# Kernel tuning notes

Measured on AMD Instinct MI355X. Metric: run time of the kernel, lower is better.

## Reference

```python
import jax, jax.numpy as jnp
import numpy as np

S = 1024      # sequence length
V = 32000     # vocab size
H = 1024      # hidden_dim
A = 128       # attn_size (module default)


def lstm_cell(x, h, c, Wih, Whh, b):
    # torch LSTM gate order: i, f, g, o
    g = x @ Wih.T + h @ Whh.T + b
    i, f, gg, o = jnp.split(g, 4)
    c = jax.nn.sigmoid(f) * c + jax.nn.sigmoid(i) * jnp.tanh(gg)
    h = jax.nn.sigmoid(o) * jnp.tanh(c)
    return h, c


def setup_inputs() -> dict:
    key = jax.random.key(0)
    ks = jax.random.split(key, 16)
    p = lambda k, shape: (jax.random.normal(k, shape, jnp.float32) * 0.02)
    return {
        'input_seq': jax.random.randint(ks[0], (S,), 0, V),
        'gold_seq': jax.random.randint(ks[1], (S,), 0, V),
        'embed': p(ks[2], (V, H)),
        'enc_Wih': p(ks[3], (4 * H, H)),
        'enc_Whh': p(ks[4], (4 * H, H)),
        'enc_b': jnp.zeros((4 * H,), jnp.float32),   # b_ih + b_hh combined
        'dec_Wih': p(ks[5], (4 * H, 2 * H)),          # decoder input = [prev, context]
        'dec_Whh': p(ks[6], (4 * H, H)),
        'dec_b': jnp.zeros((4 * H,), jnp.float32),
        'U_w': p(ks[7], (A, H)), 'U_b': jnp.zeros((A,), jnp.float32),
        'Wa_w': p(ks[8], (A, H)), 'Wa_b': jnp.zeros((A,), jnp.float32),
        'Va_w': p(ks[9], (1, A)), 'Va_b': jnp.zeros((1,), jnp.float32),
        'out_w': p(ks[10], (V, H)), 'out_b': jnp.zeros((V,), jnp.float32),
    }


def reference(input_seq, gold_seq, embed, enc_Wih, enc_Whh, enc_b,
              dec_Wih, dec_Whh, dec_b, U_w, U_b, Wa_w, Wa_b, Va_w, Va_b,
              out_w, out_b):
    Hd = embed.shape[1]
    x_emb = embed[input_seq]  # (S, H)

    def enc_step(carry, x):
        h, c = carry
        h, c = lstm_cell(x, h, c, enc_Wih, enc_Whh, enc_b)
        return (h, c), h

    zero = jnp.zeros((Hd,), x_emb.dtype)
    (h0, c0), enc_out = jax.lax.scan(enc_step, (zero, zero), x_emb)  # enc_out: (S, H)

    U_enc = enc_out @ U_w.T + U_b  # (S, A), hidden-independent part of additive attention

    # teacher forcing: prev_0 = zeros, prev_i = embed(gold[i-1]); relu applied each step
    prev = jnp.concatenate([jnp.zeros((1, Hd), x_emb.dtype), embed[gold_seq[:-1]]], axis=0)
    prev = jax.nn.relu(prev)  # (S, H)

    def dec_step(carry, p):
        h, c = carry
        # additive attention scores: V(tanh(U(enc) + W(h)))  -> (S, 1)
        scores = jnp.tanh(U_enc + h @ Wa_w.T + Wa_b) @ Va_w.T + Va_b
        # faithful to nn.Softmax() on a (S,1) tensor: torch picks dim=1 -> all ones
        w = jax.nn.softmax(scores, axis=1)  # (S, 1), == ones
        context = w[:, 0] @ enc_out         # (H,) == sum of encoder outputs
        x = jnp.concatenate([p, context])   # (2H,)
        h, c = lstm_cell(x, h, c, dec_Wih, dec_Whh, dec_b)
        logits = h @ out_w.T + out_b        # (V,)
        return (h, c), (logits, jnp.argmax(logits))

    _, (preds, idxs) = jax.lax.scan(dec_step, (h0, c0), prev)
    return preds, idxs  # (S, V) float logits, (S,) predicted ids
```

## Files before the change

kernel.cpp:

```cpp
#include <hip/hip_runtime.h>
#include <math.h>


#define S_LEN 1024
#define HDIM  1024
#define VDIM  32000

typedef float f4 __attribute__((ext_vector_type(4)));

__device__ __forceinline__ void agent_storef(float* p, float v) {
    __hip_atomic_store(p, v, __ATOMIC_RELAXED, __HIP_MEMORY_SCOPE_AGENT);
}
__device__ __forceinline__ float sigmoidf_(float x) {
    return 1.0f / (1.0f + expf(-x));
}
__device__ __forceinline__ void llc_load_4x4(const float* p, f4& a, f4& b,
                                             f4& c, f4& d) {
    asm volatile(
        "global_load_dwordx4 %0, %4, off sc0 sc1\n\t"
        "global_load_dwordx4 %1, %4, off offset:1024 sc0 sc1\n\t"
        "global_load_dwordx4 %2, %4, off offset:2048 sc0 sc1\n\t"
        "global_load_dwordx4 %3, %4, off offset:3072 sc0 sc1\n\t"
        "s_waitcnt vmcnt(0)"
        : "=&v"(a), "=&v"(b), "=&v"(c), "=&v"(d)
        : "v"(p) : "memory");
}
__device__ __forceinline__ int swz(int s) {
    return (s & ~7) | ((s ^ (s >> 3)) & 7);
}

template<int MODE>
__global__ __launch_bounds__(256)
void gemm_nt(const float* __restrict__ A, int lda,
             const float* __restrict__ B, int ldb,
             const float* __restrict__ bias,
             float* __restrict__ C, int ldc,
             const float* __restrict__ embed,
             const int* __restrict__ gidx,
             int M, int N, int K)
{
    __shared__ float As[16][128];
    __shared__ float Bs[16][128];

    const int tid = threadIdx.x;
    const int m0 = blockIdx.y * 128;
    const int n0 = blockIdx.x * 128;

    float acc[8][8];
#pragma unroll
    for (int r = 0; r < 8; ++r)
#pragma unroll
        for (int c = 0; c < 8; ++c) acc[r][c] = 0.0f;

    const int ty = tid >> 4;
    const int tx = tid & 15;

    for (int k0 = 0; k0 < K; k0 += 16) {
#pragma unroll
        for (int q = 0; q < 2; ++q) {
            int id = tid * 2 + q;
            int m  = id >> 2;
            int c4 = (id & 3) * 4;
            float4 v;
            if (MODE == 0) {
                v = *(const float4*)(A + (size_t)(m0 + m) * lda + k0 + c4);
            } else if (MODE == 1) {
                int row = gidx[m0 + m];
                v = *(const float4*)(embed + (size_t)row * HDIM + k0 + c4);
            } else {
                int mg = m0 + m;
                if (mg == 0) {
                    v = make_float4(0.f, 0.f, 0.f, 0.f);
                } else {
                    int row = gidx[mg - 1];
                    v = *(const float4*)(embed + (size_t)row * HDIM + k0 + c4);
                    v.x = fmaxf(v.x, 0.f); v.y = fmaxf(v.y, 0.f);
                    v.z = fmaxf(v.z, 0.f); v.w = fmaxf(v.w, 0.f);
                }
            }
            As[c4 + 0][m] = v.x; As[c4 + 1][m] = v.y;
            As[c4 + 2][m] = v.z; As[c4 + 3][m] = v.w;
        }
#pragma unroll
        for (int q = 0; q < 2; ++q) {
            int id = tid * 2 + q;
            int n  = id >> 2;
            int c4 = (id & 3) * 4;
            float4 v = *(const float4*)(B + (size_t)(n0 + n) * ldb + k0 + c4);
            Bs[c4 + 0][n] = v.x; Bs[c4 + 1][n] = v.y;
            Bs[c4 + 2][n] = v.z; Bs[c4 + 3][n] = v.w;
        }
        __syncthreads();

#pragma unroll
        for (int k = 0; k < 16; ++k) {
            float4 a0 = *(const float4*)&As[k][ty * 8];
            float4 a1 = *(const float4*)&As[k][ty * 8 + 4];
            float4 b0 = *(const float4*)&Bs[k][tx * 8];
            float4 b1 = *(const float4*)&Bs[k][tx * 8 + 4];
            float av[8] = {a0.x,a0.y,a0.z,a0.w,a1.x,a1.y,a1.z,a1.w};
            float bv[8] = {b0.x,b0.y,b0.z,b0.w,b1.x,b1.y,b1.z,b1.w};
#pragma unroll
            for (int r = 0; r < 8; ++r)
#pragma unroll
                for (int c = 0; c < 8; ++c)
                    acc[r][c] = fmaf(av[r], bv[c], acc[r][c]);
        }
        __syncthreads();
    }

    const int mbase = m0 + ty * 8;
    const int nbase = n0 + tx * 8;
#pragma unroll
    for (int r = 0; r < 8; ++r) {
        float4 o0, o1;
        o0.x = acc[r][0] + bias[nbase + 0];
        o0.y = acc[r][1] + bias[nbase + 1];
        o0.z = acc[r][2] + bias[nbase + 2];
        o0.w = acc[r][3] + bias[nbase + 3];
        o1.x = acc[r][4] + bias[nbase + 4];
        o1.y = acc[r][5] + bias[nbase + 5];
        o1.z = acc[r][6] + bias[nbase + 6];
        o1.w = acc[r][7] + bias[nbase + 7];
        *(float4*)(C + (size_t)(mbase + r) * ldc + nbase)     = o0;
        *(float4*)(C + (size_t)(mbase + r) * ldc + nbase + 4) = o1;
    }
}

__global__ __launch_bounds__(512, 2)
void lstm_seq(const float* __restrict__ Whh,
              const float* __restrict__ G,
              const float* __restrict__ h_init,
              const float* __restrict__ c_init,
              float* __restrict__ h_out,
              float* __restrict__ c_fin,
              float* __restrict__ csum_out,
              int slen)
{
    __shared__ f4 hbuf[256];
    const int tid = threadIdx.x;
    const int g   = blockIdx.x;
    const int wv  = tid >> 6;
    const int lg  = tid & 63;
    const int j   = g * 8 + wv;

    f4 W[4][4];
#pragma unroll
    for (int q = 0; q < 4; ++q)
#pragma unroll
        for (int i = 0; i < 4; ++i)
            W[q][i] = *(const f4*)(Whh + (size_t)(j + q * HDIM) * HDIM
                                   + 4 * lg + 256 * i);

    float c = 0.0f, csum = 0.0f;
    if (lg == 0) c = c_init[j];

    float gnow = G[(size_t)(lg & 3) * HDIM + j];

    for (int t = 0; t < slen; ++t) {
#pragma unroll
        for (int q = 0; q < 4; ++q)
#pragma unroll
            for (int i = 0; i < 4; ++i)
                asm volatile("" : "+v"(W[q][i]));

        const float* hp = (t == 0) ? h_init : (h_out + (size_t)(t - 1) * HDIM);

        if (wv == 0) {
            f4 a, b, cc, d;
            const float* p = hp + 4 * lg;
            for (;;) {
                llc_load_4x4(p, a, b, cc, d);
                float s0 = (a.x + a.y) + (a.z + a.w);
                float s1 = (b.x + b.y) + (b.z + b.w);
                float s2 = (cc.x + cc.y) + (cc.z + cc.w);
                float s3 = (d.x + d.y) + (d.z + d.w);
                float s  = (s0 + s1) + (s2 + s3);
                if (!__any(s != s)) break;
                __builtin_amdgcn_s_sleep(1);
            }
            hbuf[swz(lg)]       = a;
            hbuf[swz(64 + lg)]  = b;
            hbuf[swz(128 + lg)] = cc;
            hbuf[swz(192 + lg)] = d;
        }
        __syncthreads();

        int tn = (t + 1 < slen) ? (t + 1) : t;
        float gnext = G[(size_t)tn * (4 * HDIM) + (lg & 3) * HDIM + j];

        f4 h0 = hbuf[swz(lg)];
        f4 h1 = hbuf[swz(64 + lg)];
        f4 h2 = hbuf[swz(128 + lg)];
        f4 h3 = hbuf[swz(192 + lg)];
        float p0 = 0.f, p1 = 0.f, p2 = 0.f, p3 = 0.f;
        f4 hv;
#pragma unroll
        for (int i = 0; i < 4; ++i) {
            hv = (i == 0) ? h0 : (i == 1) ? h1 : (i == 2) ? h2 : h3;
            p0 = fmaf(W[0][i].x, hv.x, fmaf(W[0][i].y, hv.y,
                 fmaf(W[0][i].z, hv.z, fmaf(W[0][i].w, hv.w, p0))));
            p1 = fmaf(W[1][i].x, hv.x, fmaf(W[1][i].y, hv.y,
                 fmaf(W[1][i].z, hv.z, fmaf(W[1][i].w, hv.w, p1))));
            p2 = fmaf(W[2][i].x, hv.x, fmaf(W[2][i].y, hv.y,
                 fmaf(W[2][i].z, hv.z, fmaf(W[2][i].w, hv.w, p2))));
            p3 = fmaf(W[3][i].x, hv.x, fmaf(W[3][i].y, hv.y,
                 fmaf(W[3][i].z, hv.z, fmaf(W[3][i].w, hv.w, p3))));
        }

        float t01 = __shfl_xor((lg & 1) ? p0 : p1, 1);
        float s01 = ((lg & 1) ? p1 : p0) + t01;
        float t23 = __shfl_xor((lg & 1) ? p2 : p3, 1);
        float s23 = ((lg & 1) ? p3 : p2) + t23;
        float tq  = __shfl_xor((lg & 2) ? s01 : s23, 2);
        float s   = ((lg & 2) ? s23 : s01) + tq;
        s += __shfl_xor(s, 4);
        s += __shfl_xor(s, 8);
        s += __shfl_xor(s, 16);
        s += __shfl_xor(s, 32);

        float pre = s + gnow;
        float act = ((lg & 3) == 2) ? tanhf(pre) : sigmoidf_(pre);
        float a1 = __shfl(act, 1);
        float a2 = __shfl(act, 2);
        float a3 = __shfl(act, 3);

        if (lg == 0) {
            c = a1 * c + act * a2;
            float h = a3 * tanhf(c);
            csum += h;
            agent_storef(h_out + (size_t)t * HDIM + j, h);
        }
        gnow = gnext;

        __syncthreads();
    }

    if (lg == 0) {
        if (c_fin)    c_fin[j]    = c;
        if (csum_out) csum_out[j] = csum;
    }
}

__global__ __launch_bounds__(256)
void ctx_bias_k(const float* __restrict__ dec_Wih,
                const float* __restrict__ dec_b,
                const float* __restrict__ ctx,
                float* __restrict__ out)
{
    const int wv = threadIdx.x >> 6;
    const int lane = threadIdx.x & 63;
    const int r = blockIdx.x * 4 + wv;
    const float* wr = dec_Wih + (size_t)r * (2 * HDIM) + HDIM;
    float s = 0.f;
    for (int k = lane; k < HDIM; k += 64) s += wr[k] * ctx[k];
#pragma unroll
    for (int off = 32; off > 0; off >>= 1) s += __shfl_xor(s, off);
    if (lane == 0) out[r] = s + dec_b[r];
}

__global__ __launch_bounds__(256)
void argmax_k(const float* __restrict__ logits, float* __restrict__ out_idx)
{
    __shared__ float bv[256];
    __shared__ int   bidx[256];
    const int row = blockIdx.x;
    const int tid = threadIdx.x;
    const float* p = logits + (size_t)row * VDIM;
    float best = -INFINITY;
    int   bi   = 0;
    for (int v = tid; v < VDIM; v += 256) {
        float x = p[v];
        if (x > best) { best = x; bi = v; }
    }
    bv[tid] = best; bidx[tid] = bi;
    __syncthreads();
    for (int s = 128; s > 0; s >>= 1) {
        if (tid < s) {
            if (bv[tid + s] > bv[tid] ||
                (bv[tid + s] == bv[tid] && bidx[tid + s] < bidx[tid])) {
                bv[tid] = bv[tid + s];
                bidx[tid] = bidx[tid + s];
            }
        }
        __syncthreads();
    }
    if (tid == 0) out_idx[row] = (float)bidx[0];
}

extern "C" void kernel_launch(void* const* d_in, const int* in_sizes, int n_in,
                              void* d_out, int out_size, void* d_ws, size_t ws_size,
                              hipStream_t stream)
{
    (void)in_sizes; (void)n_in; (void)out_size; (void)ws_size;

    const int*   input_seq = (const int*)d_in[0];
    const int*   gold_seq  = (const int*)d_in[1];
    const float* embed     = (const float*)d_in[2];
    const float* enc_Wih   = (const float*)d_in[3];
    const float* enc_Whh   = (const float*)d_in[4];
    const float* enc_b     = (const float*)d_in[5];
    const float* dec_Wih   = (const float*)d_in[6];
    const float* dec_Whh   = (const float*)d_in[7];
    const float* dec_b     = (const float*)d_in[8];
    const float* out_w     = (const float*)d_in[15];
    const float* out_b     = (const float*)d_in[16];

    float* out = (float*)d_out;

    float* G_enc = out;
    float* G_dec = out + 4194304;

    float* zerovec   = (float*)d_ws + 256;
    float* c0        = zerovec + 1024;
    float* ctx       = c0 + 1024;
    float* ctxb      = ctx + 1024;
    float* enc_out   = ctxb + 4096;
    float* dec_h     = enc_out + 1048576;

    hipMemsetAsync(d_ws, 0, 5120, stream);
    hipMemsetAsync(enc_out, 0xFF, (size_t)S_LEN * HDIM * 4, stream);
    hipMemsetAsync(dec_h,   0xFF, (size_t)S_LEN * HDIM * 4, stream);

    dim3 blk(256);

    gemm_nt<1><<<dim3(32, 8), blk, 0, stream>>>(
        nullptr, 0, enc_Wih, HDIM, enc_b, G_enc, 4 * HDIM,
        embed, input_seq, S_LEN, 4 * HDIM, HDIM);

    lstm_seq<<<128, dim3(512), 0, stream>>>(
        enc_Whh, G_enc, zerovec, zerovec, enc_out, c0, ctx, S_LEN);

    ctx_bias_k<<<1024, blk, 0, stream>>>(dec_Wih, dec_b, ctx, ctxb);

    gemm_nt<2><<<dim3(32, 8), blk, 0, stream>>>(
        nullptr, 0, dec_Wih, 2 * HDIM, ctxb, G_dec, 4 * HDIM,
        embed, gold_seq, S_LEN, 4 * HDIM, HDIM);

    lstm_seq<<<128, dim3(512), 0, stream>>>(
        dec_Whh, G_dec, enc_out + (size_t)(S_LEN - 1) * HDIM, c0,
        dec_h, nullptr, nullptr, S_LEN);

    gemm_nt<0><<<dim3(VDIM / 128, 8), blk, 0, stream>>>(
        dec_h, HDIM, out_w, HDIM, out_b, out, VDIM,
        nullptr, nullptr, S_LEN, VDIM, HDIM);

    argmax_k<<<1024, blk, 0, stream>>>(out, out + (size_t)S_LEN * VDIM);
}
```

Measured before the change: 5.335 ms.

## Replicate LSTM hidden state across eight copies to spread cross-block polling

Each block now publishes its 8 hidden values as two 16-byte stores into one of eight replicated h buffers. Blocks poll the replica chosen by their block index modulo 8, instead of all 128 blocks spinning on the same h_out row. This is meant to cut contention on those shared cache lines and replace the per-lane relaxed atomic stores with batched stores. In exchange it adds a 32 MB NaN-fill memset before each LSTM pass and eight times the store traffic per step. Each replica write also happens one barrier later, at the start of the next step.

After: 5.406 ms. No clear change (+1.3%).

```diff
diff --git a/kernel.cpp b/kernel.cpp
--- a/kernel.cpp
+++ b/kernel.cpp
@@ -8,9 +8,6 @@
 
 typedef float f4 __attribute__((ext_vector_type(4)));
 
-__device__ __forceinline__ void agent_storef(float* p, float v) {
-    __hip_atomic_store(p, v, __ATOMIC_RELAXED, __HIP_MEMORY_SCOPE_AGENT);
-}
 __device__ __forceinline__ float sigmoidf_(float x) {
     return 1.0f / (1.0f + expf(-x));
 }
@@ -24,6 +21,10 @@
         "s_waitcnt vmcnt(0)"
         : "=&v"(a), "=&v"(b), "=&v"(c), "=&v"(d)
         : "v"(p) : "memory");
+}
+__device__ __forceinline__ void llc_store4(float* p, f4 v) {
+    asm volatile("global_store_dwordx4 %0, %1, off sc0 sc1"
+                 :: "v"(p), "v"(v) : "memory");
 }
 __device__ __forceinline__ int swz(int s) {
     return (s & ~7) | ((s ^ (s >> 3)) & 7);
@@ -133,16 +134,19 @@
               const float* __restrict__ h_init,
               const float* __restrict__ c_init,
               float* __restrict__ h_out,
+              float* __restrict__ hrep,
               float* __restrict__ c_fin,
               float* __restrict__ csum_out,
               int slen)
 {
     __shared__ f4 hbuf[256];
+    __shared__ __align__(16) float hout8[8];
     const int tid = threadIdx.x;
     const int g   = blockIdx.x;
     const int wv  = tid >> 6;
     const int lg  = tid & 63;
     const int j   = g * 8 + wv;
+    const int rep = g & 7;
 
     f4 W[4][4];
 #pragma unroll
@@ -164,25 +168,38 @@
             for (int i = 0; i < 4; ++i)
                 asm volatile("" : "+v"(W[q][i]));
 
-        const float* hp = (t == 0) ? h_init : (h_out + (size_t)(t - 1) * HDIM);
-
         if (wv == 0) {
             f4 a, b, cc, d;
-            const float* p = hp + 4 * lg;
-            for (;;) {
-                llc_load_4x4(p, a, b, cc, d);
-                float s0 = (a.x + a.y) + (a.z + a.w);
-                float s1 = (b.x + b.y) + (b.z + b.w);
-                float s2 = (cc.x + cc.y) + (cc.z + cc.w);
-                float s3 = (d.x + d.y) + (d.z + d.w);
-                float s  = (s0 + s1) + (s2 + s3);
-                if (!__any(s != s)) break;
-                __builtin_amdgcn_s_sleep(1);
+            if (t == 0) {
+                const float* p = h_init + 4 * lg;
+                a  = *(const f4*)(p);
+                b  = *(const f4*)(p + 256);
+                cc = *(const f4*)(p + 512);
+                d  = *(const f4*)(p + 768);
+            } else {
+                const float* p = hrep + ((size_t)rep * S_LEN + (t - 1)) * HDIM
+                                 + 4 * lg;
+                for (;;) {
+                    llc_load_4x4(p, a, b, cc, d);
+                    float s0 = (a.x + a.y) + (a.z + a.w);
+                    float s1 = (b.x + b.y) + (b.z + b.w);
+                    float s2 = (cc.x + cc.y) + (cc.z + cc.w);
+                    float s3 = (d.x + d.y) + (d.z + d.w);
+                    float s  = (s0 + s1) + (s2 + s3);
+                    if (!__any(s != s)) break;
+                    __builtin_amdgcn_s_sleep(1);
+                }
             }
             hbuf[swz(lg)]       = a;
             hbuf[swz(64 + lg)]  = b;
             hbuf[swz(128 + lg)] = cc;
             hbuf[swz(192 + lg)] = d;
+        } else if (wv == 1 && t > 0 && lg < 16) {
+            int r    = lg >> 1;
+            int half = lg & 1;
+            f4 v = *(const f4*)&hout8[half * 4];
+            llc_store4(hrep + ((size_t)r * S_LEN + (t - 1)) * HDIM
+                       + g * 8 + half * 4, v);
         }
         __syncthreads();
 
@@ -229,7 +246,8 @@
             c = a1 * c + act * a2;
             float h = a3 * tanhf(c);
             csum += h;
-            agent_storef(h_out + (size_t)t * HDIM + j, h);
+            hout8[wv] = h;
+            h_out[(size_t)t * HDIM + j] = h;
         }
         gnow = gnext;
 
@@ -310,6 +328,7 @@
 
     float* G_enc = out;
     float* G_dec = out + 4194304;
+    float* hrep  = out + 8388608;
 
     float* zerovec   = (float*)d_ws + 256;
     float* c0        = zerovec + 1024;
@@ -319,8 +338,7 @@
     float* dec_h     = enc_out + 1048576;
 
     hipMemsetAsync(d_ws, 0, 5120, stream);
-    hipMemsetAsync(enc_out, 0xFF, (size_t)S_LEN * HDIM * 4, stream);
-    hipMemsetAsync(dec_h,   0xFF, (size_t)S_LEN * HDIM * 4, stream);
+    hipMemsetAsync(hrep, 0xFF, (size_t)8 * S_LEN * HDIM * 4, stream);
 
     dim3 blk(256);
 
@@ -329,7 +347,7 @@
         embed, input_seq, S_LEN, 4 * HDIM, HDIM);
 
     lstm_seq<<<128, dim3(512), 0, stream>>>(
-        enc_Whh, G_enc, zerovec, zerovec, enc_out, c0, ctx, S_LEN);
+        enc_Whh, G_enc, zerovec, zerovec, enc_out, hrep, c0, ctx, S_LEN);
 
     ctx_bias_k<<<1024, blk, 0, stream>>>(dec_Wih, dec_b, ctx, ctxb);
 
@@ -337,9 +355,11 @@
         nullptr, 0, dec_Wih, 2 * HDIM, ctxb, G_dec, 4 * HDIM,
         embed, gold_seq, S_LEN, 4 * HDIM, HDIM);
 
+    hipMemsetAsync(hrep, 0xFF, (size_t)8 * S_LEN * HDIM * 4, stream);
+
     lstm_seq<<<128, dim3(512), 0, stream>>>(
         dec_Whh, G_dec, enc_out + (size_t)(S_LEN - 1) * HDIM, c0,
-        dec_h, nullptr, nullptr, S_LEN);
+        dec_h, hrep, nullptr, nullptr, S_LEN);
 
     gemm_nt<0><<<dim3(VDIM / 128, 8), blk, 0, stream>>>(
         dec_h, HDIM, out_w, HDIM, out_b, out, VDIM,
```

## Fuse input GEMMs and output GEMM with recurrent LSTM kernels via flag polling

Applied to the files above, without the earlier changes.

Merges the encoder input-projection GEMM, the decoder input-projection GEMM and the encoder LSTM recurrence into one launch. The LSTM blocks poll NaN-initialised G_enc entries, so the recurrence can start before the whole projection finishes. Likewise, the decoder LSTM and the vocabulary output GEMM share one launch, with GEMM tiles polling the decoder hidden rows they need, so the large logits GEMM overlaps the serial recurrence. The ctx bias is moved from the G_dec GEMM epilogue into the decoder LSTM. The main risks are deadlock or starvation if the polling blocks are not co-resident, extra memsets, and contention between the GEMM tiles and the latency-critical LSTM blocks.

Result: slower. 7.027 ms (+31.7%).

```diff
diff --git a/kernel.cpp b/kernel.cpp
--- a/kernel.cpp
+++ b/kernel.cpp
@@ -5,6 +5,7 @@
 #define S_LEN 1024
 #define HDIM  1024
 #define VDIM  32000
+#define GDEC_OFF 28573696
 
 typedef float f4 __attribute__((ext_vector_type(4)));
 
@@ -13,6 +14,13 @@
 }
 __device__ __forceinline__ float sigmoidf_(float x) {
     return 1.0f / (1.0f + expf(-x));
+}
+__device__ __forceinline__ float llc_loadf(const float* p) {
+    float v;
+    asm volatile("global_load_dword %0, %1, off sc0 sc1\n\t"
+                 "s_waitcnt vmcnt(0)"
+                 : "=v"(v) : "v"(p) : "memory");
+    return v;
 }
 __device__ __forceinline__ void llc_load_4x4(const float* p, f4& a, f4& b,
                                              f4& c, f4& d) {
@@ -25,118 +33,34 @@
         : "=&v"(a), "=&v"(b), "=&v"(c), "=&v"(d)
         : "v"(p) : "memory");
 }
+__device__ __forceinline__ void llc_store4(float* p, f4 v) {
+    asm volatile("global_store_dwordx4 %0, %1, off sc0 sc1"
+                 :: "v"(p), "v"(v) : "memory");
+}
+__device__ __forceinline__ bool any_nan16(f4 a, f4 b, f4 c, f4 d) {
+    float s0 = (a.x + a.y) + (a.z + a.w);
+    float s1 = (b.x + b.y) + (b.z + b.w);
+    float s2 = (c.x + c.y) + (c.z + c.w);
+    float s3 = (d.x + d.y) + (d.z + d.w);
+    float s  = (s0 + s1) + (s2 + s3);
+    return s != s;
+}
 __device__ __forceinline__ int swz(int s) {
     return (s & ~7) | ((s ^ (s >> 3)) & 7);
 }
 
-template<int MODE>
-__global__ __launch_bounds__(256)
-void gemm_nt(const float* __restrict__ A, int lda,
-             const float* __restrict__ B, int ldb,
-             const float* __restrict__ bias,
-             float* __restrict__ C, int ldc,
-             const float* __restrict__ embed,
-             const int* __restrict__ gidx,
-             int M, int N, int K)
-{
-    __shared__ float As[16][128];
-    __shared__ float Bs[16][128];
-
-    const int tid = threadIdx.x;
-    const int m0 = blockIdx.y * 128;
-    const int n0 = blockIdx.x * 128;
-
-    float acc[8][8];
-#pragma unroll
-    for (int r = 0; r < 8; ++r)
-#pragma unroll
-        for (int c = 0; c < 8; ++c) acc[r][c] = 0.0f;
-
-    const int ty = tid >> 4;
-    const int tx = tid & 15;
-
-    for (int k0 = 0; k0 < K; k0 += 16) {
-#pragma unroll
-        for (int q = 0; q < 2; ++q) {
-            int id = tid * 2 + q;
-            int m  = id >> 2;
-            int c4 = (id & 3) * 4;
-            float4 v;
-            if (MODE == 0) {
-                v = *(const float4*)(A + (size_t)(m0 + m) * lda + k0 + c4);
-            } else if (MODE == 1) {
-                int row = gidx[m0 + m];
-                v = *(const float4*)(embed + (size_t)row * HDIM + k0 + c4);
-            } else {
-                int mg = m0 + m;
-                if (mg == 0) {
-                    v = make_float4(0.f, 0.f, 0.f, 0.f);
-                } else {
-                    int row = gidx[mg - 1];
-                    v = *(const float4*)(embed + (size_t)row * HDIM + k0 + c4);
-                    v.x = fmaxf(v.x, 0.f); v.y = fmaxf(v.y, 0.f);
-                    v.z = fmaxf(v.z, 0.f); v.w = fmaxf(v.w, 0.f);
-                }
-            }
-            As[c4 + 0][m] = v.x; As[c4 + 1][m] = v.y;
-            As[c4 + 2][m] = v.z; As[c4 + 3][m] = v.w;
-        }
-#pragma unroll
-        for (int q = 0; q < 2; ++q) {
-            int id = tid * 2 + q;
-            int n  = id >> 2;
-            int c4 = (id & 3) * 4;
-            float4 v = *(const float4*)(B + (size_t)(n0 + n) * ldb + k0 + c4);
-            Bs[c4 + 0][n] = v.x; Bs[c4 + 1][n] = v.y;
-            Bs[c4 + 2][n] = v.z; Bs[c4 + 3][n] = v.w;
-        }
-        __syncthreads();
-
-#pragma unroll
-        for (int k = 0; k < 16; ++k) {
-            float4 a0 = *(const float4*)&As[k][ty * 8];
-            float4 a1 = *(const float4*)&As[k][ty * 8 + 4];
-            float4 b0 = *(const float4*)&Bs[k][tx * 8];
-            float4 b1 = *(const float4*)&Bs[k][tx * 8 + 4];
-            float av[8] = {a0.x,a0.y,a0.z,a0.w,a1.x,a1.y,a1.z,a1.w};
-            float bv[8] = {b0.x,b0.y,b0.z,b0.w,b1.x,b1.y,b1.z,b1.w};
-#pragma unroll
-            for (int r = 0; r < 8; ++r)
-#pragma unroll
-                for (int c = 0; c < 8; ++c)
-                    acc[r][c] = fmaf(av[r], bv[c], acc[r][c]);
-        }
-        __syncthreads();
-    }
-
-    const int mbase = m0 + ty * 8;
-    const int nbase = n0 + tx * 8;
-#pragma unroll
-    for (int r = 0; r < 8; ++r) {
-        float4 o0, o1;
-        o0.x = acc[r][0] + bias[nbase + 0];
-        o0.y = acc[r][1] + bias[nbase + 1];
-        o0.z = acc[r][2] + bias[nbase + 2];
-        o0.w = acc[r][3] + bias[nbase + 3];
-        o1.x = acc[r][4] + bias[nbase + 4];
-        o1.y = acc[r][5] + bias[nbase + 5];
-        o1.z = acc[r][6] + bias[nbase + 6];
-        o1.w = acc[r][7] + bias[nbase + 7];
-        *(float4*)(C + (size_t)(mbase + r) * ldc + nbase)     = o0;
-        *(float4*)(C + (size_t)(mbase + r) * ldc + nbase + 4) = o1;
-    }
-}
-
-__global__ __launch_bounds__(512, 2)
-void lstm_seq(const float* __restrict__ Whh,
-              const float* __restrict__ G,
-              const float* __restrict__ h_init,
-              const float* __restrict__ c_init,
-              float* __restrict__ h_out,
-              float* __restrict__ c_fin,
-              float* __restrict__ csum_out,
-              int slen)
-{
+template<int GMODE>
+__device__ void lstm_block(const float* __restrict__ Whh,
+                           const float* __restrict__ G,
+                           const float* __restrict__ gctx_vec,
+                           const float* __restrict__ h_init,
+                           const float* __restrict__ c_init,
+                           float* __restrict__ h_out,
+                           float* __restrict__ c_fin,
+                           float* __restrict__ csum_out,
+                           int slen)
+{
+    __builtin_amdgcn_s_setprio(1);
     __shared__ f4 hbuf[256];
     const int tid = threadIdx.x;
     const int g   = blockIdx.x;
@@ -155,7 +79,21 @@
     float c = 0.0f, csum = 0.0f;
     if (lg == 0) c = c_init[j];
 
-    float gnow = G[(size_t)(lg & 3) * HDIM + j];
+    float gctx = 0.0f;
+    if (GMODE == 1) gctx = gctx_vec[(size_t)(lg & 3) * HDIM + j];
+
+    float gnow;
+    {
+        const float* gp = G + (size_t)(lg & 3) * HDIM + j;
+        if (GMODE == 0) {
+            gnow = llc_loadf(gp);
+            while (__any(gnow != gnow)) {
+                if (gnow != gnow) { __builtin_amdgcn_s_sleep(2); gnow = llc_loadf(gp); }
+            }
+        } else {
+            gnow = *gp + gctx;
+        }
+    }
 
     for (int t = 0; t < slen; ++t) {
 #pragma unroll
@@ -171,12 +109,7 @@
             const float* p = hp + 4 * lg;
             for (;;) {
                 llc_load_4x4(p, a, b, cc, d);
-                float s0 = (a.x + a.y) + (a.z + a.w);
-                float s1 = (b.x + b.y) + (b.z + b.w);
-                float s2 = (cc.x + cc.y) + (cc.z + cc.w);
-                float s3 = (d.x + d.y) + (d.z + d.w);
-                float s  = (s0 + s1) + (s2 + s3);
-                if (!__any(s != s)) break;
+                if (!__any(any_nan16(a, b, cc, d))) break;
                 __builtin_amdgcn_s_sleep(1);
             }
             hbuf[swz(lg)]       = a;
@@ -187,7 +120,16 @@
         __syncthreads();
 
         int tn = (t + 1 < slen) ? (t + 1) : t;
-        float gnext = G[(size_t)tn * (4 * HDIM) + (lg & 3) * HDIM + j];
+        const float* gp = G + (size_t)tn * (4 * HDIM) + (lg & 3) * HDIM + j;
+        float gnext;
+        if (GMODE == 0) {
+            gnext = llc_loadf(gp);
+            while (__any(gnext != gnext)) {
+                if (gnext != gnext) { __builtin_amdgcn_s_sleep(2); gnext = llc_loadf(gp); }
+            }
+        } else {
+            gnext = *gp + gctx;
+        }
 
         f4 h0 = hbuf[swz(lg)];
         f4 h1 = hbuf[swz(64 + lg)];
@@ -239,6 +181,167 @@
     if (lg == 0) {
         if (c_fin)    c_fin[j]    = c;
         if (csum_out) csum_out[j] = csum;
+        if (GMODE == 1)
+            agent_storef(h_out + (size_t)slen * HDIM + j, 0.0f);
+    }
+}
+
+template<int MODE>
+__device__ void gemm_tile(const float* __restrict__ A, int lda,
+                          const float* __restrict__ B, int ldb,
+                          const float* __restrict__ bias,
+                          float* __restrict__ C, int ldc,
+                          const float* __restrict__ embed,
+                          const int* __restrict__ gidx,
+                          int mt, int nt, int K,
+                          const float* __restrict__ pollbuf)
+{
+    __shared__ float As[16][128];
+    __shared__ float Bs[16][128];
+    const int tid = threadIdx.x;
+    const int m0 = mt * 128;
+    const int n0 = nt * 128;
+
+    if (MODE == 0) {
+        if (mt < 7) {
+            if (tid == 0) {
+                const float* p = pollbuf + (size_t)(m0 + 128) * HDIM;
+                float v = llc_loadf(p);
+                while (v != v) { __builtin_amdgcn_s_sleep(16); v = llc_loadf(p); }
+            }
+        } else {
+            if (tid < 64) {
+                const float* p = pollbuf + (size_t)S_LEN * HDIM + 4 * tid;
+                f4 a, b, cc, d;
+                for (;;) {
+                    llc_load_4x4(p, a, b, cc, d);
+                    if (!__any(any_nan16(a, b, cc, d))) break;
+                    __builtin_amdgcn_s_sleep(16);
+                }
+            }
+        }
+        __syncthreads();
+    }
+
+    float acc[8][4];
+#pragma unroll
+    for (int r = 0; r < 8; ++r)
+#pragma unroll
+        for (int cc = 0; cc < 4; ++cc) acc[r][cc] = 0.0f;
+
+    const int ty = tid >> 5;
+    const int tx = tid & 31;
+    const int lm = tid >> 2;
+    const int c4 = (tid & 3) * 4;
+
+    for (int k0 = 0; k0 < K; k0 += 16) {
+        float4 v;
+        if (MODE == 0) {
+            v = *(const float4*)(A + (size_t)(m0 + lm) * lda + k0 + c4);
+        } else if (MODE == 1) {
+            int row = gidx[m0 + lm];
+            v = *(const float4*)(embed + (size_t)row * HDIM + k0 + c4);
+        } else {
+            int mg = m0 + lm;
+            if (mg == 0) {
+                v = make_float4(0.f, 0.f, 0.f, 0.f);
+            } else {
+                int row = gidx[mg - 1];
+                v = *(const float4*)(embed + (size_t)row * HDIM + k0 + c4);
+                v.x = fmaxf(v.x, 0.f); v.y = fmaxf(v.y, 0.f);
+                v.z = fmaxf(v.z, 0.f); v.w = fmaxf(v.w, 0.f);
+            }
+        }
+        As[c4 + 0][lm] = v.x; As[c4 + 1][lm] = v.y;
+        As[c4 + 2][lm] = v.z; As[c4 + 3][lm] = v.w;
+
+        float4 w = *(const float4*)(B + (size_t)(n0 + lm) * ldb + k0 + c4);
+        Bs[c4 + 0][lm] = w.x; Bs[c4 + 1][lm] = w.y;
+        Bs[c4 + 2][lm] = w.z; Bs[c4 + 3][lm] = w.w;
+        __syncthreads();
+
+#pragma unroll
+        for (int k = 0; k < 16; ++k) {
+            f4 a0 = *(const f4*)&As[k][ty * 8];
+            f4 a1 = *(const f4*)&As[k][ty * 8 + 4];
+            f4 b  = *(const f4*)&Bs[k][tx * 4];
+            float av[8] = {a0.x,a0.y,a0.z,a0.w,a1.x,a1.y,a1.z,a1.w};
+            float bv[4] = {b.x,b.y,b.z,b.w};
+#pragma unroll
+            for (int r = 0; r < 8; ++r)
+#pragma unroll
+                for (int cc = 0; cc < 4; ++cc)
+                    acc[r][cc] = fmaf(av[r], bv[cc], acc[r][cc]);
+        }
+        __syncthreads();
+    }
+
+    const int mbase = m0 + ty * 8;
+    const int nbase = n0 + tx * 4;
+#pragma unroll
+    for (int r = 0; r < 8; ++r) {
+        f4 o;
+        o.x = acc[r][0] + ((MODE == 2) ? 0.f : bias[nbase + 0]);
+        o.y = acc[r][1] + ((MODE == 2) ? 0.f : bias[nbase + 1]);
+        o.z = acc[r][2] + ((MODE == 2) ? 0.f : bias[nbase + 2]);
+        o.w = acc[r][3] + ((MODE == 2) ? 0.f : bias[nbase + 3]);
+        float* cp = C + (size_t)(mbase + r) * ldc + nbase;
+        if (MODE == 1) llc_store4(cp, o);
+        else           *(f4*)cp = o;
+    }
+}
+
+__global__ __launch_bounds__(512, 1)
+void enc_phase(const float* __restrict__ embed,
+               const int* __restrict__ input_seq,
+               const int* __restrict__ gold_seq,
+               const float* __restrict__ enc_Wih,
+               const float* __restrict__ enc_b,
+               const float* __restrict__ dec_Wih,
+               const float* __restrict__ enc_Whh,
+               float* __restrict__ G_enc,
+               float* __restrict__ G_dec,
+               const float* __restrict__ zerovec,
+               float* __restrict__ enc_out,
+               float* __restrict__ c0,
+               float* __restrict__ ctx)
+{
+    const int bid = blockIdx.x;
+    if (bid < 128) {
+        lstm_block<0>(enc_Whh, G_enc, nullptr, zerovec, zerovec,
+                      enc_out, c0, ctx, S_LEN);
+    } else if (bid < 384) {
+        int q = bid - 128;
+        gemm_tile<1>(nullptr, 0, enc_Wih, HDIM, enc_b, G_enc, 4 * HDIM,
+                     embed, input_seq, q >> 5, q & 31, HDIM, nullptr);
+    } else {
+        int q = bid - 384;
+        gemm_tile<2>(nullptr, 0, dec_Wih, 2 * HDIM, nullptr, G_dec, 4 * HDIM,
+                     embed, gold_seq, q >> 5, q & 31, HDIM, nullptr);
+    }
+}
+
+__global__ __launch_bounds__(512, 1)
+void dec_phase(const float* __restrict__ dec_Whh,
+               const float* __restrict__ G_dec,
+               const float* __restrict__ ctxb,
+               const float* __restrict__ h_init,
+               const float* __restrict__ c0,
+               float* __restrict__ dec_h,
+               const float* __restrict__ out_w,
+               const float* __restrict__ out_b,
+               float* __restrict__ out)
+{
+    const int bid = blockIdx.x;
+    if (bid < 128) {
+        lstm_block<1>(dec_Whh, G_dec, ctxb, h_init, c0,
+                      dec_h, nullptr, nullptr, S_LEN);
+    } else {
+        int q = bid - 128;
+        int mt = q / 250;
+        int nt = q % 250;
+        gemm_tile<0>(dec_h, HDIM, out_w, HDIM, out_b, out, VDIM,
+                     nullptr, nullptr, mt, nt, HDIM, dec_h);
     }
 }
 
@@ -309,41 +412,29 @@
     float* out = (float*)d_out;
 
     float* G_enc = out;
-    float* G_dec = out + 4194304;
-
-    float* zerovec   = (float*)d_ws + 256;
-    float* c0        = zerovec + 1024;
-    float* ctx       = c0 + 1024;
-    float* ctxb      = ctx + 1024;
-    float* enc_out   = ctxb + 4096;
-    float* dec_h     = enc_out + 1048576;
+    float* G_dec = out + GDEC_OFF;
+
+    float* zerovec = (float*)d_ws + 256;
+    float* c0      = zerovec + 1024;
+    float* ctx     = c0 + 1024;
+    float* ctxb    = ctx + 1024;
+    float* enc_out = ctxb + 4096;
+    float* dec_h   = enc_out + 1048576;
 
     hipMemsetAsync(d_ws, 0, 5120, stream);
     hipMemsetAsync(enc_out, 0xFF, (size_t)S_LEN * HDIM * 4, stream);
-    hipMemsetAsync(dec_h,   0xFF, (size_t)S_LEN * HDIM * 4, stream);
-
-    dim3 blk(256);
-
-    gemm_nt<1><<<dim3(32, 8), blk, 0, stream>>>(
-        nullptr, 0, enc_Wih, HDIM, enc_b, G_enc, 4 * HDIM,
-        embed, input_seq, S_LEN, 4 * HDIM, HDIM);
-
-    lstm_seq<<<128, dim3(512), 0, stream>>>(
-        enc_Whh, G_enc, zerovec, zerovec, enc_out, c0, ctx, S_LEN);
-
-    ctx_bias_k<<<1024, blk, 0, stream>>>(dec_Wih, dec_b, ctx, ctxb);
-
-    gemm_nt<2><<<dim3(32, 8), blk, 0, stream>>>(
-        nullptr, 0, dec_Wih, 2 * HDIM, ctxb, G_dec, 4 * HDIM,
-        embed, gold_seq, S_LEN, 4 * HDIM, HDIM);
-
-    lstm_seq<<<128, dim3(512), 0, stream>>>(
-        dec_Whh, G_dec, enc_out + (size_t)(S_LEN - 1) * HDIM, c0,
-        dec_h, nullptr, nullptr, S_LEN);
-
-    gemm_nt<0><<<dim3(VDIM / 128, 8), blk, 0, stream>>>(
-        dec_h, HDIM, out_w, HDIM, out_b, out, VDIM,
-        nullptr, nullptr, S_LEN, VDIM, HDIM);
-
-    argmax_k<<<1024, blk, 0, stream>>>(out, out + (size_t)S_LEN * VDIM);
-}
+    hipMemsetAsync(dec_h,   0xFF, (size_t)(S_LEN + 1) * HDIM * 4, stream);
+    hipMemsetAsync(G_enc,   0xFF, (size_t)S_LEN * 4 * HDIM * 4, stream);
+
+    enc_phase<<<640, 512, 0, stream>>>(
+        embed, input_seq, gold_seq, enc_Wih, enc_b, dec_Wih, enc_Whh,
+        G_enc, G_dec, zerovec, enc_out, c0, ctx);
+
+    ctx_bias_k<<<1024, 256, 0, stream>>>(dec_Wih, dec_b, ctx, ctxb);
+
+    dec_phase<<<2128, 512, 0, stream>>>(
+        dec_Whh, G_dec, ctxb, enc_out + (size_t)(S_LEN - 1) * HDIM, c0,
+        dec_h, out_w, out_b, out);
+
+    argmax_k<<<1024, 256, 0, stream>>>(out, out + (size_t)S_LEN * VDIM);
+}
```
